# Kernel optimization log

Hardware: AMD Instinct MI355X
Metric: run time of the kernel (lower is better)

The kernel has to match this reference:

```python
import jax, jax.numpy as jnp
import numpy as np

B, H1, H2, D, C = 4096, 32, 32, 32, 64


def setup_inputs() -> dict:
    key = jax.random.key(0)
    k1, k2, k3 = jax.random.split(key, 3)
    x = jax.random.normal(k1, (B, H1, D), dtype=jnp.float32)
    y = jax.random.normal(k2, (B, H2, D), dtype=jnp.float32)
    # glorot-uniform-ish kernel of shape (compress_dim, H1, H2)
    limit = float(np.sqrt(6.0 / (H1 + H2)))
    kernel = jax.random.uniform(k3, (C, H1, H2), dtype=jnp.float32,
                                minval=-limit, maxval=limit)
    return {"x": x, "y": y, "kernel": kernel}


def reference(x, y, kernel):
    # Original math: outer[b,i,j,d] = x[b,i,d]*y[b,j,d];
    # output_mat[b,c,d] = sum_{i,j} outer[b,i,j,d] * kernel[c,i,j]
    # Expressed as a fused bilinear contraction (avoids the [B,H1,H2,D] tensor):
    # first fold kernel into y per compress channel, then contract with x.
    t = jnp.einsum('cij,bjd->bcid', kernel, y)       # [B,C,H1,D]
    output_mat = jnp.einsum('bid,bcid->bcd', x, t)   # [B,C,D]
    final_output = jnp.sum(output_mat, axis=-1)      # [B,C]
    return (output_mat, final_output)
```

## Files before the change

### kernel.cpp

```cpp
#include <hip/hip_runtime.h>
#include <hip/hip_fp16.h>


typedef __attribute__((ext_vector_type(8))) _Float16 half8;
typedef __attribute__((ext_vector_type(2))) __fp16 fp16x2;
typedef __attribute__((ext_vector_type(4))) float f32x4;
typedef __attribute__((ext_vector_type(8))) short short8;

__device__ __forceinline__ unsigned int dup_h(float f) {
    union { fp16x2 h; unsigned int u; } w;
    w.h = __builtin_amdgcn_cvt_pkrtz(f, f);
    return w.u;
}
__device__ __forceinline__ fp16x2 pk2(float a, float b) {
    return __builtin_amdgcn_cvt_pkrtz(a, b);
}

__global__ __launch_bounds__(256) void kswz_kernel(const float* __restrict__ kern,
                                                   unsigned short* __restrict__ kswz) {
    int idx  = blockIdx.x * 256 + threadIdx.x;
    int lane = idx & 63;
    int nt   = (idx >> 6) & 3;
    int s    = idx >> 8;
    int c    = nt * 16 + (lane & 15);
    int jb   = (lane >> 4) * 8;
    const float* src = kern + c * 1024 + s * 32 + jb;
    union { half8 h; short8 s8; } v;
#pragma unroll
    for (int t = 0; t < 8; ++t) v.h[t] = (_Float16)src[t];
    *(short8*)(kswz + (size_t)idx * 8) = v.s8;
}

__device__ __forceinline__ void gld_lds16(const void* g, void* l) {
    __builtin_amdgcn_global_load_lds(
        (const __attribute__((address_space(1))) unsigned int*)g,
        (__attribute__((address_space(3))) unsigned int*)l, 16, 0, 0);
}

__global__ __launch_bounds__(256, 2) void cin_main(const float* __restrict__ x,
                                                   const float* __restrict__ y,
                                                   const unsigned short* __restrict__ kswz,
                                                   float* __restrict__ out_mat,
                                                   float* __restrict__ out_fin) {
    __shared__ __align__(16) unsigned short kb[3][8192];
    __shared__ __align__(16) float xb[3][1024];

    const int tid  = threadIdx.x;
    const int wave = tid >> 6;
    const int lane = tid & 63;
    const int quad = lane >> 4;
    const int n16  = lane & 15;
    const int b_blk = blockIdx.x * 8;
    const int cq0   = blockIdx.x & 7;

    const int xbb = tid >> 5;
    const int xii = (tid >> 3) & 3;
    const int xd4 = tid & 7;

    auto issue_chunk = [&](int ci, int slot) {
#pragma unroll
        for (int r = 0; r < 4; ++r)
            gld_lds16(kswz + (size_t)ci * 8192 + (r * 256 + tid) * 8,
                      &kb[slot][r * 2048 + wave * 512]);
        gld_lds16(x + (size_t)(b_blk + xbb) * 1024 + ci * 128 + xii * 32 + xd4 * 4,
                  &xb[slot][wave * 256]);
    };

    issue_chunk(cq0, 0);
    issue_chunk((cq0 + 1) & 7, 1);

    const int b0 = b_blk + wave * 2;
    fp16x2 yv2[4][4];
#pragma unroll
    for (int mt = 0; mt < 4; ++mt) {
        const int b = b0 + (mt >> 1);
        const int d = n16 + 16 * (mt & 1);
        const float* yp = y + (size_t)b * 1024 + (quad * 8) * 32 + d;
#pragma unroll
        for (int p = 0; p < 4; ++p)
            yv2[mt][p] = pk2(yp[(2 * p) * 32], yp[(2 * p + 1) * 32]);
    }

    f32x4 acc[4][4];
#pragma unroll
    for (int mt = 0; mt < 4; ++mt)
#pragma unroll
        for (int nt = 0; nt < 4; ++nt) acc[mt][nt] = (f32x4){0.f, 0.f, 0.f, 0.f};

#pragma unroll
    for (int p8 = 0; p8 < 8; ++p8) {
        if (p8 < 7) asm volatile("s_waitcnt vmcnt(5)" ::: "memory");
        else        asm volatile("s_waitcnt vmcnt(0)" ::: "memory");
        __builtin_amdgcn_s_barrier();
        __builtin_amdgcn_sched_barrier(0);

        if (p8 < 6) issue_chunk((cq0 + p8 + 2) & 7, (p8 + 2) % 3);

        const unsigned short* kbase = &kb[p8 % 3][0];
        const float*          xbase = &xb[p8 % 3][0];

        __builtin_amdgcn_s_setprio(1);
#pragma unroll
        for (int k = 0; k < 4; ++k) {
            half8 bf[4];
#pragma unroll
            for (int nt = 0; nt < 4; ++nt)
                bf[nt] = *(const half8*)(kbase + ((k * 4 + nt) * 64 + lane) * 8);
#pragma unroll
            for (int mt = 0; mt < 4; ++mt) {
                float xf = xbase[(wave * 2 + (mt >> 1)) * 128 + k * 32 + n16 + 16 * (mt & 1)];
                union { unsigned int u; fp16x2 h; } xv;
                xv.u = dup_h(xf);
                union { half8 h8; fp16x2 h2[4]; } af;
#pragma unroll
                for (int p = 0; p < 4; ++p) af.h2[p] = xv.h * yv2[mt][p];
#pragma unroll
                for (int nt = 0; nt < 4; ++nt)
                    acc[mt][nt] = __builtin_amdgcn_mfma_f32_16x16x32_f16(
                        af.h8, bf[nt], acc[mt][nt], 0, 0, 0);
            }
        }
        __builtin_amdgcn_s_setprio(0);
    }

#pragma unroll
    for (int mt = 0; mt < 4; ++mt) {
        const int b = b0 + (mt >> 1);
        const int dbase = 16 * (mt & 1) + quad * 4;
#pragma unroll
        for (int nt = 0; nt < 4; ++nt) {
            const int c = nt * 16 + n16;
            *(f32x4*)(out_mat + (size_t)b * 2048 + c * 32 + dbase) = acc[mt][nt];
        }
    }

#pragma unroll
    for (int a = 0; a < 2; ++a) {
        const int b = b0 + a;
#pragma unroll
        for (int nt = 0; nt < 4; ++nt) {
            float f = 0.f;
#pragma unroll
            for (int t = 0; t < 4; ++t) f += acc[2 * a][nt][t] + acc[2 * a + 1][nt][t];
            f += __shfl_xor(f, 16);
            f += __shfl_xor(f, 32);
            if (lane < 16) out_fin[(size_t)b * 64 + nt * 16 + n16] = f;
        }
    }
}

extern "C" void kernel_launch(void* const* d_in, const int* in_sizes, int n_in,
                              void* d_out, int out_size, void* d_ws, size_t ws_size,
                              hipStream_t stream) {
    const float* x    = (const float*)d_in[0];
    const float* y    = (const float*)d_in[1];
    const float* kern = (const float*)d_in[2];
    float* out_mat = (float*)d_out;
    float* out_fin = (float*)d_out + 4096 * 64 * 32;
    unsigned short* kswz = (unsigned short*)d_ws;

    kswz_kernel<<<32, 256, 0, stream>>>(kern, kswz);
    cin_main<<<512, 256, 0, stream>>>(x, y, kswz, out_mat, out_fin);
}
```

Baseline: 100.7 us.

## Fuse kernel fp16 swizzle into main kernel via register-staged loads

Removes the separate pre-pass that converted and swizzled the kernel tensor to fp16 in workspace. Each block now loads fp32 kernel rows into registers, converts them to fp16 and writes the swizzled layout to a double-buffered LDS slot, with a pipeline restructured around this. This saves one launch and the workspace round trip. In exchange every block reloads and converts twice as many kernel bytes, adds register pressure, and needs an extra barrier per iteration.

Measured after the change: 106.2 us. +5.5%, slower.

```diff
diff --git a/kernel.cpp b/kernel.cpp
--- a/kernel.cpp
+++ b/kernel.cpp
@@ -15,22 +15,6 @@
 __device__ __forceinline__ fp16x2 pk2(float a, float b) {
     return __builtin_amdgcn_cvt_pkrtz(a, b);
 }
-
-__global__ __launch_bounds__(256) void kswz_kernel(const float* __restrict__ kern,
-                                                   unsigned short* __restrict__ kswz) {
-    int idx  = blockIdx.x * 256 + threadIdx.x;
-    int lane = idx & 63;
-    int nt   = (idx >> 6) & 3;
-    int s    = idx >> 8;
-    int c    = nt * 16 + (lane & 15);
-    int jb   = (lane >> 4) * 8;
-    const float* src = kern + c * 1024 + s * 32 + jb;
-    union { half8 h; short8 s8; } v;
-#pragma unroll
-    for (int t = 0; t < 8; ++t) v.h[t] = (_Float16)src[t];
-    *(short8*)(kswz + (size_t)idx * 8) = v.s8;
-}
-
 __device__ __forceinline__ void gld_lds16(const void* g, void* l) {
     __builtin_amdgcn_global_load_lds(
         (const __attribute__((address_space(1))) unsigned int*)g,
@@ -39,10 +23,10 @@
 
 __global__ __launch_bounds__(256, 2) void cin_main(const float* __restrict__ x,
                                                    const float* __restrict__ y,
-                                                   const unsigned short* __restrict__ kswz,
+                                                   const float* __restrict__ kern,
                                                    float* __restrict__ out_mat,
                                                    float* __restrict__ out_fin) {
-    __shared__ __align__(16) unsigned short kb[3][8192];
+    __shared__ __align__(16) unsigned short kb[2][8192];
     __shared__ __align__(16) float xb[3][1024];
 
     const int tid  = threadIdx.x;
@@ -53,21 +37,39 @@
     const int b_blk = blockIdx.x * 8;
     const int cq0   = blockIdx.x & 7;
 
-    const int xbb = tid >> 5;
-    const int xii = (tid >> 3) & 3;
-    const int xd4 = tid & 7;
+    const int xbb = tid >> 5, xii = (tid >> 3) & 3, xd4 = tid & 7;
 
-    auto issue_chunk = [&](int ci, int slot) {
+    const float* bsrc = kern + (size_t)(wave * 16 + n16) * 1024 + quad * 8;
+
+    float4 breg[2][8];
+
+    auto issue_B = [&](int ci, int par) {
+        const float* s0 = bsrc + ci * 128;
 #pragma unroll
-        for (int r = 0; r < 4; ++r)
-            gld_lds16(kswz + (size_t)ci * 8192 + (r * 256 + tid) * 8,
-                      &kb[slot][r * 2048 + wave * 512]);
+        for (int r = 0; r < 4; ++r) {
+            breg[par][2 * r]     = *(const float4*)(s0 + r * 32);
+            breg[par][2 * r + 1] = *(const float4*)(s0 + r * 32 + 4);
+        }
+    };
+    auto issue_x = [&](int ci, int slot) {
         gld_lds16(x + (size_t)(b_blk + xbb) * 1024 + ci * 128 + xii * 32 + xd4 * 4,
                   &xb[slot][wave * 256]);
     };
+    auto write_B = [&](int par, int slot) {
+#pragma unroll
+        for (int r = 0; r < 4; ++r) {
+            union { half8 h; short8 s; } v;
+#pragma unroll
+            for (int t = 0; t < 4; ++t) {
+                v.h[t]     = (_Float16)breg[par][2 * r][t];
+                v.h[4 + t] = (_Float16)breg[par][2 * r + 1][t];
+            }
+            *(short8*)(&kb[slot][r * 2048 + tid * 8]) = v.s;
+        }
+    };
 
-    issue_chunk(cq0, 0);
-    issue_chunk((cq0 + 1) & 7, 1);
+    issue_B(cq0, 0);           issue_x(cq0, 0);
+    issue_B((cq0 + 1) & 7, 1); issue_x((cq0 + 1) & 7, 1);
 
     const int b0 = b_blk + wave * 2;
     fp16x2 yv2[4][4];
@@ -87,17 +89,20 @@
 #pragma unroll
         for (int nt = 0; nt < 4; ++nt) acc[mt][nt] = (f32x4){0.f, 0.f, 0.f, 0.f};
 
+    write_B(0, 0);
+    asm volatile("s_waitcnt lgkmcnt(0)" ::: "memory");
+    __builtin_amdgcn_s_barrier();
+    __builtin_amdgcn_sched_barrier(0);
+
 #pragma unroll
-    for (int p8 = 0; p8 < 8; ++p8) {
-        if (p8 < 7) asm volatile("s_waitcnt vmcnt(5)" ::: "memory");
-        else        asm volatile("s_waitcnt vmcnt(0)" ::: "memory");
-        __builtin_amdgcn_s_barrier();
-        __builtin_amdgcn_sched_barrier(0);
+    for (int p = 0; p < 8; ++p) {
+        if (p <= 5) { issue_B((cq0 + p + 2) & 7, p & 1); issue_x((cq0 + p + 2) & 7, (p + 2) % 3); }
+        if (p <= 5)      asm volatile("s_waitcnt vmcnt(9)" ::: "memory");
+        else if (p == 6) asm volatile("s_waitcnt vmcnt(0)" ::: "memory");
+        if (p <= 6) write_B((p + 1) & 1, (p + 1) & 1);
 
-        if (p8 < 6) issue_chunk((cq0 + p8 + 2) & 7, (p8 + 2) % 3);
-
-        const unsigned short* kbase = &kb[p8 % 3][0];
-        const float*          xbase = &xb[p8 % 3][0];
+        const unsigned short* kbase = &kb[p & 1][0];
+        const float*          xbase = &xb[p % 3][0];
 
         __builtin_amdgcn_s_setprio(1);
 #pragma unroll
@@ -113,7 +118,7 @@
                 xv.u = dup_h(xf);
                 union { half8 h8; fp16x2 h2[4]; } af;
 #pragma unroll
-                for (int p = 0; p < 4; ++p) af.h2[p] = xv.h * yv2[mt][p];
+                for (int pq = 0; pq < 4; ++pq) af.h2[pq] = xv.h * yv2[mt][pq];
 #pragma unroll
                 for (int nt = 0; nt < 4; ++nt)
                     acc[mt][nt] = __builtin_amdgcn_mfma_f32_16x16x32_f16(
@@ -121,6 +126,10 @@
             }
         }
         __builtin_amdgcn_s_setprio(0);
+
+        asm volatile("s_waitcnt lgkmcnt(0)" ::: "memory");
+        __builtin_amdgcn_s_barrier();
+        __builtin_amdgcn_sched_barrier(0);
     }
 
 #pragma unroll
@@ -157,8 +166,7 @@
     const float* kern = (const float*)d_in[2];
     float* out_mat = (float*)d_out;
     float* out_fin = (float*)d_out + 4096 * 64 * 32;
-    unsigned short* kswz = (unsigned short*)d_ws;
+    (void)d_ws; (void)ws_size;
 
-    kswz_kernel<<<32, 256, 0, stream>>>(kern, kswz);
-    cin_main<<<512, 256, 0, stream>>>(x, y, kswz, out_mat, out_fin);
+    cin_main<<<512, 256, 0, stream>>>(x, y, kern, out_mat, out_fin);
 }
```

## Split compress channels across wave pairs and double the grid

Applied to the files above, without the earlier changes.

Each block now covers 4 batch rows instead of 8. Pairs of waves split the 64 compress channels into halves, so each wave keeps half as many accumulators, and the grid grows to 1024 blocks. The x tile is loaded in a separate double-buffered stream every two k-chunks, with retuned vmcnt waits. The aim is more parallelism and lower register pressure per wave. In exchange, kernel chunks are re-fetched into LDS twice as often per output row.

After: 104.1 us. +3.4%, slower.

```diff
diff --git a/kernel.cpp b/kernel.cpp
--- a/kernel.cpp
+++ b/kernel.cpp
@@ -15,6 +15,11 @@
 __device__ __forceinline__ fp16x2 pk2(float a, float b) {
     return __builtin_amdgcn_cvt_pkrtz(a, b);
 }
+__device__ __forceinline__ void gld_lds16(const void* g, void* l) {
+    __builtin_amdgcn_global_load_lds(
+        (const __attribute__((address_space(1))) unsigned int*)g,
+        (__attribute__((address_space(3))) unsigned int*)l, 16, 0, 0);
+}
 
 __global__ __launch_bounds__(256) void kswz_kernel(const float* __restrict__ kern,
                                                    unsigned short* __restrict__ kswz) {
@@ -31,45 +36,41 @@
     *(short8*)(kswz + (size_t)idx * 8) = v.s8;
 }
 
-__device__ __forceinline__ void gld_lds16(const void* g, void* l) {
-    __builtin_amdgcn_global_load_lds(
-        (const __attribute__((address_space(1))) unsigned int*)g,
-        (__attribute__((address_space(3))) unsigned int*)l, 16, 0, 0);
-}
-
 __global__ __launch_bounds__(256, 2) void cin_main(const float* __restrict__ x,
                                                    const float* __restrict__ y,
                                                    const unsigned short* __restrict__ kswz,
                                                    float* __restrict__ out_mat,
                                                    float* __restrict__ out_fin) {
     __shared__ __align__(16) unsigned short kb[3][8192];
-    __shared__ __align__(16) float xb[3][1024];
+    __shared__ __align__(16) float xb[2][1024];
 
-    const int tid  = threadIdx.x;
-    const int wave = tid >> 6;
-    const int lane = tid & 63;
-    const int quad = lane >> 4;
-    const int n16  = lane & 15;
-    const int b_blk = blockIdx.x * 8;
-    const int cq0   = blockIdx.x & 7;
+    const int tid   = threadIdx.x;
+    const int wave  = tid >> 6;
+    const int lane  = tid & 63;
+    const int quad  = lane >> 4;
+    const int n16   = lane & 15;
+    const int chalf = wave & 1;
+    const int bp    = wave >> 1;
+    const int b_blk = blockIdx.x * 4;
+    const int cq0   = (blockIdx.x & 3) * 2;
 
-    const int xbb = tid >> 5;
-    const int xii = (tid >> 3) & 3;
-    const int xd4 = tid & 7;
-
-    auto issue_chunk = [&](int ci, int slot) {
+    auto issue_B = [&](int ci, int slot) {
 #pragma unroll
         for (int r = 0; r < 4; ++r)
             gld_lds16(kswz + (size_t)ci * 8192 + (r * 256 + tid) * 8,
                       &kb[slot][r * 2048 + wave * 512]);
-        gld_lds16(x + (size_t)(b_blk + xbb) * 1024 + ci * 128 + xii * 32 + xd4 * 4,
+    };
+    auto issue_X = [&](int P, int slot) {
+        const int rowbase = ((cq0 + 2 * P) & 7) * 4;
+        gld_lds16(x + (size_t)(b_blk + wave) * 1024 + (rowbase + (lane >> 3)) * 32 + (lane & 7) * 4,
                   &xb[slot][wave * 256]);
     };
 
-    issue_chunk(cq0, 0);
-    issue_chunk((cq0 + 1) & 7, 1);
+    issue_B(cq0, 0);
+    issue_X(0, 0);
+    issue_B((cq0 + 1) & 7, 1);
 
-    const int b0 = b_blk + wave * 2;
+    const int b0 = b_blk + bp * 2;
     fp16x2 yv2[4][4];
 #pragma unroll
     for (int mt = 0; mt < 4; ++mt) {
@@ -81,41 +82,44 @@
             yv2[mt][p] = pk2(yp[(2 * p) * 32], yp[(2 * p + 1) * 32]);
     }
 
-    f32x4 acc[4][4];
+    f32x4 acc[4][2];
 #pragma unroll
     for (int mt = 0; mt < 4; ++mt)
 #pragma unroll
-        for (int nt = 0; nt < 4; ++nt) acc[mt][nt] = (f32x4){0.f, 0.f, 0.f, 0.f};
+        for (int nt = 0; nt < 2; ++nt) acc[mt][nt] = (f32x4){0.f, 0.f, 0.f, 0.f};
 
 #pragma unroll
-    for (int p8 = 0; p8 < 8; ++p8) {
-        if (p8 < 7) asm volatile("s_waitcnt vmcnt(5)" ::: "memory");
-        else        asm volatile("s_waitcnt vmcnt(0)" ::: "memory");
+    for (int p = 0; p < 8; ++p) {
+        if (p == 7)       asm volatile("s_waitcnt vmcnt(0)" ::: "memory");
+        else if (p & 1)   asm volatile("s_waitcnt vmcnt(5)" ::: "memory");
+        else              asm volatile("s_waitcnt vmcnt(4)" ::: "memory");
         __builtin_amdgcn_s_barrier();
         __builtin_amdgcn_sched_barrier(0);
 
-        if (p8 < 6) issue_chunk((cq0 + p8 + 2) & 7, (p8 + 2) % 3);
+        if (p <= 5) issue_B((cq0 + p + 2) & 7, (p + 2) % 3);
+        if (p <= 4 && (p & 1) == 0) issue_X(p / 2 + 1, (p / 2 + 1) & 1);
 
-        const unsigned short* kbase = &kb[p8 % 3][0];
-        const float*          xbase = &xb[p8 % 3][0];
+        const unsigned short* kbase = &kb[p % 3][0];
+        const float*          xbase = &xb[(p / 2) & 1][0];
 
         __builtin_amdgcn_s_setprio(1);
 #pragma unroll
         for (int k = 0; k < 4; ++k) {
-            half8 bf[4];
+            half8 bf[2];
 #pragma unroll
-            for (int nt = 0; nt < 4; ++nt)
-                bf[nt] = *(const half8*)(kbase + ((k * 4 + nt) * 64 + lane) * 8);
+            for (int nt = 0; nt < 2; ++nt)
+                bf[nt] = *(const half8*)(kbase + ((k * 4 + chalf * 2 + nt) * 64 + lane) * 8);
 #pragma unroll
             for (int mt = 0; mt < 4; ++mt) {
-                float xf = xbase[(wave * 2 + (mt >> 1)) * 128 + k * 32 + n16 + 16 * (mt & 1)];
+                float xf = xbase[(bp * 2 + (mt >> 1)) * 256 + ((p & 1) * 4 + k) * 32 +
+                                 n16 + 16 * (mt & 1)];
                 union { unsigned int u; fp16x2 h; } xv;
                 xv.u = dup_h(xf);
                 union { half8 h8; fp16x2 h2[4]; } af;
 #pragma unroll
-                for (int p = 0; p < 4; ++p) af.h2[p] = xv.h * yv2[mt][p];
+                for (int pq = 0; pq < 4; ++pq) af.h2[pq] = xv.h * yv2[mt][pq];
 #pragma unroll
-                for (int nt = 0; nt < 4; ++nt)
+                for (int nt = 0; nt < 2; ++nt)
                     acc[mt][nt] = __builtin_amdgcn_mfma_f32_16x16x32_f16(
                         af.h8, bf[nt], acc[mt][nt], 0, 0, 0);
             }
@@ -128,8 +132,8 @@
         const int b = b0 + (mt >> 1);
         const int dbase = 16 * (mt & 1) + quad * 4;
 #pragma unroll
-        for (int nt = 0; nt < 4; ++nt) {
-            const int c = nt * 16 + n16;
+        for (int nt = 0; nt < 2; ++nt) {
+            const int c = chalf * 32 + nt * 16 + n16;
             *(f32x4*)(out_mat + (size_t)b * 2048 + c * 32 + dbase) = acc[mt][nt];
         }
     }
@@ -138,13 +142,13 @@
     for (int a = 0; a < 2; ++a) {
         const int b = b0 + a;
 #pragma unroll
-        for (int nt = 0; nt < 4; ++nt) {
+        for (int nt = 0; nt < 2; ++nt) {
             float f = 0.f;
 #pragma unroll
             for (int t = 0; t < 4; ++t) f += acc[2 * a][nt][t] + acc[2 * a + 1][nt][t];
             f += __shfl_xor(f, 16);
             f += __shfl_xor(f, 32);
-            if (lane < 16) out_fin[(size_t)b * 64 + nt * 16 + n16] = f;
+            if (lane < 16) out_fin[(size_t)b * 64 + chalf * 32 + nt * 16 + n16] = f;
         }
     }
 }
@@ -160,5 +164,5 @@
     unsigned short* kswz = (unsigned short*)d_ws;
 
     kswz_kernel<<<32, 256, 0, stream>>>(kern, kswz);
-    cin_main<<<512, 256, 0, stream>>>(x, y, kswz, out_mat, out_fin);
+    cin_main<<<1024, 256, 0, stream>>>(x, y, kswz, out_mat, out_fin);
 }
```
